# Optimization experiments

Hardware: AMD Instinct MI355X
Metric: run time of the kernel (lower is better)

The kernel has to match this reference:

```python
import jax, jax.numpy as jnp
import numpy as np

BLOCK_SIZE = 4096
EMBED_SIZE = 1024
HEAD_SIZE = 128


def setup_inputs() -> dict:
    key = jax.random.key(0)
    kx, kq, kk, kv = jax.random.split(key, 4)
    B, T = 8, BLOCK_SIZE
    x = jax.random.normal(kx, (B, T, EMBED_SIZE), dtype=jnp.float32)
    # nn.Linear(embed, head, bias=False): weight (head, embed); y = x @ W.T
    scale = 1.0 / np.sqrt(EMBED_SIZE)
    Wq = jax.random.uniform(kq, (HEAD_SIZE, EMBED_SIZE), dtype=jnp.float32, minval=-scale, maxval=scale)
    Wk = jax.random.uniform(kk, (HEAD_SIZE, EMBED_SIZE), dtype=jnp.float32, minval=-scale, maxval=scale)
    Wv = jax.random.uniform(kv, (HEAD_SIZE, EMBED_SIZE), dtype=jnp.float32, minval=-scale, maxval=scale)
    return {"x": x, "Wq": Wq, "Wk": Wk, "Wv": Wv}


def reference(x, Wq, Wk, Wv):
    B, T, C = x.shape
    q = jnp.einsum('btc,hc->bth', x, Wq)  # (B,T,H)
    k = jnp.einsum('btc,hc->bth', x, Wk)
    v = jnp.einsum('btc,hc->bth', x, Wv)
    scale = jnp.asarray(Wq.shape[0], x.dtype) ** -0.5
    wei = jnp.einsum('bth,bsh->bts', q, k) * scale  # (B,T,T)
    causal = jnp.tril(jnp.ones((T, T), dtype=bool))
    wei = jnp.where(causal, wei, -jnp.inf)
    wei = jax.nn.softmax(wei, axis=-1)
    out = jnp.einsum('bts,bsh->bth', wei, v)  # (B,T,H)
    return out
```

## Files before the change

### kernel.cpp

```cpp
#include <hip/hip_runtime.h>
#include <stdint.h>

typedef unsigned short u16;
typedef __attribute__((ext_vector_type(8))) short short8;
typedef __attribute__((ext_vector_type(4))) float f32x4;

#define B_ 8
#define T_ 4096
#define C_ 1024
#define H_ 128

#if __has_builtin(__builtin_amdgcn_exp2f)
#define EXP2(x) __builtin_amdgcn_exp2f(x)
#else
#define EXP2(x) exp2f(x)
#endif

__device__ __forceinline__ u16 f2bf(float f) {
  union { float f; uint32_t u; } v; v.f = f;
  uint32_t r = v.u + 0x7fffu + ((v.u >> 16) & 1u);
  return (u16)(r >> 16);
}

__device__ __forceinline__ void gl_lds16(const u16* g, u16* l) {
  __builtin_amdgcn_global_load_lds(
      (const __attribute__((address_space(1))) void*)g,
      (__attribute__((address_space(3))) void*)l, 16, 0, 0);
}

__global__ __launch_bounds__(256) void wconv_kernel(
    const float* __restrict__ Wq, const float* __restrict__ Wk,
    const float* __restrict__ Wv, u16* __restrict__ Wb) {
  int g = (blockIdx.x * 256 + threadIdx.x) * 8;
  int head = g >> 17;
  int off  = g & 131071;
  const float* W = (head == 0) ? Wq : (head == 1) ? Wk : Wv;
  float s = (head == 0) ? 0.08838834764831845f : 1.0f;
  float4 a = *(const float4*)(W + off);
  float4 b = *(const float4*)(W + off + 4);
  u16 o[8] = {f2bf(a.x * s), f2bf(a.y * s), f2bf(a.z * s), f2bf(a.w * s),
              f2bf(b.x * s), f2bf(b.y * s), f2bf(b.z * s), f2bf(b.w * s)};
  *(uint4*)(Wb + g) = *(const uint4*)o;
}

__global__ __launch_bounds__(512) void proj_kernel(
    const float* __restrict__ x, const u16* __restrict__ Wb,
    u16* __restrict__ qo, u16* __restrict__ ko, u16* __restrict__ vto) {
  __shared__ u16 Xl[64 * 72];
  __shared__ u16 Wl[384 * 72];

  const int bm   = blockIdx.x;
  const int tid  = threadIdx.x;
  const int wave = tid >> 6;
  const int lane = tid & 63;
  const int m    = lane & 15;
  const int q4   = lane >> 4;
  const int rowg = wave & 1;
  const int colg = wave >> 1;

  f32x4 acc[12] = {};

  const int xrow = tid >> 3, xc8 = (tid & 7) * 8;

  for (int kc = 0; kc < C_; kc += 64) {
    __syncthreads();
    {
      const float* xp = x + (size_t)(bm * 64 + xrow) * C_ + kc + xc8;
      float4 a = *(const float4*)xp;
      float4 b = *(const float4*)(xp + 4);
      u16 o[8] = {f2bf(a.x), f2bf(a.y), f2bf(a.z), f2bf(a.w),
                  f2bf(b.x), f2bf(b.y), f2bf(b.z), f2bf(b.w)};
      *(uint4*)&Xl[xrow * 72 + xc8] = *(const uint4*)o;
    }
    #pragma unroll
    for (int i = 0; i < 6; ++i) {
      int g = i * 512 + tid;
      int row = g >> 3, c8 = (g & 7) * 8;
      *(uint4*)&Wl[row * 72 + c8] =
          *(const uint4*)(Wb + (size_t)row * C_ + kc + c8);
    }
    __syncthreads();

    #pragma unroll
    for (int kb = 0; kb < 2; ++kb) {
      short8 af0 = *(const short8*)&Xl[(rowg * 32 + m) * 72 + kb * 32 + q4 * 8];
      short8 af1 = *(const short8*)&Xl[(rowg * 32 + 16 + m) * 72 + kb * 32 + q4 * 8];
      #pragma unroll
      for (int nb = 0; nb < 6; ++nb) {
        short8 bf = *(const short8*)&Wl[(colg * 96 + nb * 16 + m) * 72 + kb * 32 + q4 * 8];
        acc[nb]     = __builtin_amdgcn_mfma_f32_16x16x32_bf16(af0, bf, acc[nb], 0, 0, 0);
        acc[6 + nb] = __builtin_amdgcn_mfma_f32_16x16x32_bf16(af1, bf, acc[6 + nb], 0, 0, 0);
      }
    }
  }

  #pragma unroll
  for (int half = 0; half < 2; ++half) {
    const int rowoff = rowg * 32 + half * 16 + q4 * 4;
    #pragma unroll
    for (int nb = 0; nb < 6; ++nb) {
      int col = colg * 96 + nb * 16 + m;
      f32x4 a = acc[half * 6 + nb];
      if (col < 128) {
        #pragma unroll
        for (int r = 0; r < 4; ++r)
          qo[(size_t)(bm * 64 + rowoff + r) * H_ + col] = f2bf(a[r]);
      } else if (col < 256) {
        #pragma unroll
        for (int r = 0; r < 4; ++r)
          ko[(size_t)(bm * 64 + rowoff + r) * H_ + (col - 128)] = f2bf(a[r]);
      } else {
        int b = bm >> 6;
        int t = (bm & 63) * 64 + rowoff;
        u16* vp = vto + (size_t)b * H_ * T_ + (size_t)(col - 256) * T_ + t;
        #pragma unroll
        for (int r = 0; r < 4; ++r) vp[r] = f2bf(a[r]);
      }
    }
  }
}

__global__ __launch_bounds__(256, 2) void attn_kernel(
    const u16* __restrict__ q, const u16* __restrict__ k,
    const u16* __restrict__ vt, float* __restrict__ out,
    float* __restrict__ po, float* __restrict__ pl) {
  __shared__ u16 Kl[2][64 * 128];
  __shared__ u16 Vl[2][128 * 64];
  __shared__ u16 Pl[4][16 * 72];

  const int bid   = blockIdx.x;
  const int batch = bid & 7;
  const int c     = bid >> 3;
  int qt, ck;
  if (c < 64)       { qt = 63 - (c >> 2);         ck = c & 3; }
  else if (c < 112) { qt = 47 - (c - 64) / 3;     ck = (c - 64) % 3; }
  else if (c < 144) { qt = 31 - ((c - 112) >> 1); ck = (c - 112) & 1; }
  else              { qt = 15 - (c - 144);        ck = 0; }
  const int k0   = ck * 16;
  const int kend = min(k0 + 16, qt + 1);
  const bool single = (qt < 16);

  const int tid  = threadIdx.x;
  const int wave = tid >> 6;
  const int lane = tid & 63;
  const int m    = lane & 15;
  const int q4   = lane >> 4;

  const size_t bbase = (size_t)batch * T_ * H_;
  const u16* vbase   = vt + (size_t)batch * H_ * T_;

  short8 qf[4];
  {
    const u16* qp = q + bbase + (size_t)(qt * 64 + wave * 16 + m) * H_;
    #pragma unroll
    for (int kb = 0; kb < 4; ++kb)
      qf[kb] = *(const short8*)(qp + kb * 32 + q4 * 8);
  }

  const u16* gK[4];
  const u16* gV[4];
  #pragma unroll
  for (int j = 0; j < 4; ++j) {
    int r = wave * 16 + j * 4 + (lane >> 4);
    gK[j] = k + bbase + (size_t)r * H_ + (((lane & 15) ^ (r & 7)) << 3);
    int h = wave * 32 + j * 8 + (lane >> 3);
    gV[j] = vbase + (size_t)h * T_ + (((lane & 7) ^ (h & 7)) << 3);
  }

#define STAGE(bi, KT)                                                         \
  {                                                                           \
    u16* kd = &Kl[bi][wave * 16 * 128];                                       \
    const size_t ko_ = (size_t)(KT) * (64 * H_);                              \
    _Pragma("unroll") for (int j = 0; j < 4; ++j)                             \
        gl_lds16(gK[j] + ko_, kd + j * 4 * 128);                              \
    u16* vd = &Vl[bi][wave * 32 * 64];                                        \
    const size_t vo_ = (size_t)(KT) * 64;                                     \
    _Pragma("unroll") for (int j = 0; j < 4; ++j)                             \
        gl_lds16(gV[j] + vo_, vd + j * 8 * 64);                               \
  }

  float li[4] = {0.f, 0.f, 0.f, 0.f};
  f32x4 o[8] = {};
  const float L2E = 1.4426950408889634f;
  const float NEGINF = -__builtin_inff();

  STAGE(0, k0);
  __syncthreads();
  int cur = 0;

  for (int kt = k0; kt < kend; ++kt) {
    if (kt + 1 < kend) STAGE(cur ^ 1, kt + 1);

    f32x4 s[4];
    __builtin_amdgcn_s_setprio(1);
    #pragma unroll
    for (int nb = 0; nb < 4; ++nb) {
      f32x4 a = {};
      #pragma unroll
      for (int kb = 0; kb < 4; ++kb) {
        short8 kf = *(const short8*)&Kl[cur][(nb * 16 + m) * 128 +
                                             (((kb * 4 + q4) ^ (m & 7)) << 3)];
        a = __builtin_amdgcn_mfma_f32_16x16x32_bf16(qf[kb], kf, a, 0, 0, 0);
      }
      s[nb] = a;
    }
    __builtin_amdgcn_s_setprio(0);

    if (kt == qt) {
      #pragma unroll
      for (int nb = 0; nb < 4; ++nb)
        #pragma unroll
        for (int r = 0; r < 4; ++r) {
          int col = nb * 16 + m;
          int row = wave * 16 + q4 * 4 + r;
          if (col > row) s[nb][r] = NEGINF;
        }
    }

    #pragma unroll
    for (int nb = 0; nb < 4; ++nb)
      #pragma unroll
      for (int r = 0; r < 4; ++r) {
        float p = EXP2(s[nb][r] * L2E);
        li[r] += p;
        Pl[wave][(q4 * 4 + r) * 72 + nb * 16 + m] = f2bf(p);
      }

    __asm__ __volatile__("s_waitcnt lgkmcnt(0)" ::: "memory");

    __builtin_amdgcn_s_setprio(1);
    #pragma unroll
    for (int kb2 = 0; kb2 < 2; ++kb2) {
      short8 pf = *(const short8*)&Pl[wave][m * 72 + kb2 * 32 + q4 * 8];
      #pragma unroll
      for (int nb = 0; nb < 8; ++nb) {
        short8 vf = *(const short8*)&Vl[cur][(nb * 16 + m) * 64 +
                                             (((kb2 * 4 + q4) ^ (m & 7)) << 3)];
        o[nb] = __builtin_amdgcn_mfma_f32_16x16x32_bf16(pf, vf, o[nb], 0, 0, 0);
      }
    }
    __builtin_amdgcn_s_setprio(0);

    if (kt + 1 < kend) {
      __syncthreads();
      cur ^= 1;
    }
  }

  #pragma unroll
  for (int r = 0; r < 4; ++r) {
    float t0 = li[r];
    t0 += __shfl_xor(t0, 1, 64);
    t0 += __shfl_xor(t0, 2, 64);
    t0 += __shfl_xor(t0, 4, 64);
    t0 += __shfl_xor(t0, 8, 64);
    li[r] = t0;
  }

  if (single) {
    float* op = out + bbase + (size_t)(qt * 64 + wave * 16) * H_;
    #pragma unroll
    for (int nb = 0; nb < 8; ++nb)
      #pragma unroll
      for (int r = 0; r < 4; ++r)
        op[(q4 * 4 + r) * H_ + nb * 16 + m] = o[nb][r] / li[r];
  } else {
    const size_t slot = (size_t)(batch * 64 + qt) * 4 + ck;
    float* pp = po + (slot * 64 + wave * 16) * 128;
    #pragma unroll
    for (int nb = 0; nb < 8; ++nb)
      #pragma unroll
      for (int r = 0; r < 4; ++r)
        pp[(q4 * 4 + r) * 128 + nb * 16 + m] = o[nb][r];
    if (m == 0) {
      #pragma unroll
      for (int r = 0; r < 4; ++r)
        pl[slot * 64 + wave * 16 + q4 * 4 + r] = li[r];
    }
  }
}

__global__ __launch_bounds__(256) void combine_kernel(
    const float* __restrict__ po, const float* __restrict__ pl,
    float* __restrict__ out) {
  int gid = blockIdx.x * 256 + threadIdx.x;
  int h4  = (gid & 31) * 4;
  int tt  = (gid >> 5) & 4095;
  int b   = gid >> 17;
  int qt  = tt >> 6, row = tt & 63;
  if (qt < 16) return;
  int nc = (qt >> 4) + 1;
  float4 s = {0.f, 0.f, 0.f, 0.f};
  float l = 0.f;
  for (int ck = 0; ck < nc; ++ck) {
    size_t slot = (size_t)(b * 64 + qt) * 4 + ck;
    float4 p = *(const float4*)(po + (slot * 64 + row) * 128 + h4);
    s.x += p.x; s.y += p.y; s.z += p.z; s.w += p.w;
    l += pl[slot * 64 + row];
  }
  float inv = 1.0f / l;
  float4 r; r.x = s.x * inv; r.y = s.y * inv; r.z = s.z * inv; r.w = s.w * inv;
  *(float4*)(out + ((size_t)b * T_ + tt) * H_ + h4) = r;
}

extern "C" void kernel_launch(void* const* d_in, const int* in_sizes, int n_in,
                              void* d_out, int out_size, void* d_ws,
                              size_t ws_size, hipStream_t stream) {
  const float* x  = (const float*)d_in[0];
  const float* Wq = (const float*)d_in[1];
  const float* Wk = (const float*)d_in[2];
  const float* Wv = (const float*)d_in[3];

  const size_t n = (size_t)B_ * T_ * H_;
  u16* qb  = (u16*)d_ws;
  u16* kb  = qb + n;
  u16* vtb = kb + n;
  u16* Wbb = vtb + n;
  float* po = (float*)(Wbb + 393216);
  float* pl = po + (size_t)512 * 4 * 64 * 128;

  wconv_kernel<<<dim3(192), dim3(256), 0, stream>>>(Wq, Wk, Wv, Wbb);
  proj_kernel<<<dim3(512), dim3(512), 0, stream>>>(x, Wbb, qb, kb, vtb);
  attn_kernel<<<dim3(1280), dim3(256), 0, stream>>>(qb, kb, vtb, (float*)d_out, po, pl);
  combine_kernel<<<dim3(4096), dim3(256), 0, stream>>>(po, pl, (float*)d_out);
}
```

Baseline: 308.4 us.

## Double query tile to 128 rows per block, folding log2e into Wq scale

```diff
diff --git a/kernel.cpp b/kernel.cpp
--- a/kernel.cpp
+++ b/kernel.cpp
@@ -20,6 +20,11 @@
   union { float f; uint32_t u; } v; v.f = f;
   uint32_t r = v.u + 0x7fffu + ((v.u >> 16) & 1u);
   return (u16)(r >> 16);
+}
+
+__device__ __forceinline__ u16 f2bf_rn(float f) {
+  union { float f; uint32_t u; } v; v.f = f;
+  return (u16)((v.u + 0x8000u) >> 16);
 }
 
 __device__ __forceinline__ void gl_lds16(const u16* g, u16* l) {
@@ -35,7 +40,7 @@
   int head = g >> 17;
   int off  = g & 131071;
   const float* W = (head == 0) ? Wq : (head == 1) ? Wk : Wv;
-  float s = (head == 0) ? 0.08838834764831845f : 1.0f;
+  float s = (head == 0) ? 0.12751743342f : 1.0f;
   float4 a = *(const float4*)(W + off);
   float4 b = *(const float4*)(W + off + 4);
   u16 o[8] = {f2bf(a.x * s), f2bf(a.y * s), f2bf(a.z * s), f2bf(a.w * s),
@@ -126,19 +131,20 @@
     float* __restrict__ po, float* __restrict__ pl) {
   __shared__ u16 Kl[2][64 * 128];
   __shared__ u16 Vl[2][128 * 64];
-  __shared__ u16 Pl[4][16 * 72];
+  __shared__ u16 Pl[4][2][16 * 64];
 
   const int bid   = blockIdx.x;
   const int batch = bid & 7;
   const int c     = bid >> 3;
-  int qt, ck;
-  if (c < 64)       { qt = 63 - (c >> 2);         ck = c & 3; }
-  else if (c < 112) { qt = 47 - (c - 64) / 3;     ck = (c - 64) % 3; }
-  else if (c < 144) { qt = 31 - ((c - 112) >> 1); ck = (c - 112) & 1; }
-  else              { qt = 15 - (c - 144);        ck = 0; }
+  int Q, ck;
+  if (c < 24)      { Q = 31 - c / 3;        ck = c % 3; }
+  else if (c < 40) { Q = 23 - (c - 24) / 2; ck = (c - 24) & 1; }
+  else if (c < 48) { Q = 15 - (c - 40);     ck = 0; }
+  else { int t = c - 48; int qm = 7 - (t >> 2);
+         Q = qm + (t & 3) * 8; ck = Q >> 3; }
   const int k0   = ck * 16;
-  const int kend = min(k0 + 16, qt + 1);
-  const bool single = (qt < 16);
+  const int kend = min(k0 + 16, 2 * Q + 2);
+  const bool single = (Q < 8);
 
   const int tid  = threadIdx.x;
   const int wave = tid >> 6;
@@ -149,12 +155,13 @@
   const size_t bbase = (size_t)batch * T_ * H_;
   const u16* vbase   = vt + (size_t)batch * H_ * T_;
 
-  short8 qf[4];
-  {
-    const u16* qp = q + bbase + (size_t)(qt * 64 + wave * 16 + m) * H_;
+  short8 qf[2][4];
+  #pragma unroll
+  for (int si = 0; si < 2; ++si) {
+    const u16* qp = q + bbase + (size_t)(Q * 128 + wave * 32 + si * 16 + m) * H_;
     #pragma unroll
     for (int kb = 0; kb < 4; ++kb)
-      qf[kb] = *(const short8*)(qp + kb * 32 + q4 * 8);
+      qf[si][kb] = *(const short8*)(qp + kb * 32 + q4 * 8);
   }
 
   const u16* gK[4];
@@ -179,9 +186,8 @@
         gl_lds16(gV[j] + vo_, vd + j * 8 * 64);                               \
   }
 
-  float li[4] = {0.f, 0.f, 0.f, 0.f};
-  f32x4 o[8] = {};
-  const float L2E = 1.4426950408889634f;
+  float li[2][4] = {};
+  f32x4 o[2][8] = {};
   const float NEGINF = -__builtin_inff();
 
   STAGE(0, k0);
@@ -191,52 +197,64 @@
   for (int kt = k0; kt < kend; ++kt) {
     if (kt + 1 < kend) STAGE(cur ^ 1, kt + 1);
 
-    f32x4 s[4];
+    f32x4 sv[2][4];
     __builtin_amdgcn_s_setprio(1);
     #pragma unroll
     for (int nb = 0; nb < 4; ++nb) {
-      f32x4 a = {};
+      f32x4 a0 = {}, a1 = {};
       #pragma unroll
       for (int kb = 0; kb < 4; ++kb) {
         short8 kf = *(const short8*)&Kl[cur][(nb * 16 + m) * 128 +
                                              (((kb * 4 + q4) ^ (m & 7)) << 3)];
-        a = __builtin_amdgcn_mfma_f32_16x16x32_bf16(qf[kb], kf, a, 0, 0, 0);
-      }
-      s[nb] = a;
+        a0 = __builtin_amdgcn_mfma_f32_16x16x32_bf16(qf[0][kb], kf, a0, 0, 0, 0);
+        a1 = __builtin_amdgcn_mfma_f32_16x16x32_bf16(qf[1][kb], kf, a1, 0, 0, 0);
+      }
+      sv[0][nb] = a0; sv[1][nb] = a1;
     }
     __builtin_amdgcn_s_setprio(0);
 
-    if (kt == qt) {
+    if ((kt >> 1) == Q) {
+      #pragma unroll
+      for (int si = 0; si < 2; ++si)
+        #pragma unroll
+        for (int nb = 0; nb < 4; ++nb)
+          #pragma unroll
+          for (int r = 0; r < 4; ++r) {
+            int key = ((kt & 1) << 6) + nb * 16 + m;
+            int row = wave * 32 + si * 16 + q4 * 4 + r;
+            if (key > row) sv[si][nb][r] = NEGINF;
+          }
+    }
+
+    #pragma unroll
+    for (int si = 0; si < 2; ++si)
       #pragma unroll
       for (int nb = 0; nb < 4; ++nb)
         #pragma unroll
         for (int r = 0; r < 4; ++r) {
-          int col = nb * 16 + m;
-          int row = wave * 16 + q4 * 4 + r;
-          if (col > row) s[nb][r] = NEGINF;
+          float p = EXP2(sv[si][nb][r]);
+          li[si][r] += p;
+          int rr = q4 * 4 + r;
+          Pl[wave][si][rr * 64 + (((nb * 2 + (m >> 3)) ^ (rr & 7)) << 3) +
+                       (m & 7)] = f2bf_rn(p);
         }
-    }
-
-    #pragma unroll
-    for (int nb = 0; nb < 4; ++nb)
-      #pragma unroll
-      for (int r = 0; r < 4; ++r) {
-        float p = EXP2(s[nb][r] * L2E);
-        li[r] += p;
-        Pl[wave][(q4 * 4 + r) * 72 + nb * 16 + m] = f2bf(p);
-      }
 
     __asm__ __volatile__("s_waitcnt lgkmcnt(0)" ::: "memory");
+    __builtin_amdgcn_sched_barrier(0);
 
     __builtin_amdgcn_s_setprio(1);
     #pragma unroll
     for (int kb2 = 0; kb2 < 2; ++kb2) {
-      short8 pf = *(const short8*)&Pl[wave][m * 72 + kb2 * 32 + q4 * 8];
+      short8 pf0 = *(const short8*)&Pl[wave][0][m * 64 +
+                                   (((kb2 * 4 + q4) ^ (m & 7)) << 3)];
+      short8 pf1 = *(const short8*)&Pl[wave][1][m * 64 +
+                                   (((kb2 * 4 + q4) ^ (m & 7)) << 3)];
       #pragma unroll
       for (int nb = 0; nb < 8; ++nb) {
         short8 vf = *(const short8*)&Vl[cur][(nb * 16 + m) * 64 +
                                              (((kb2 * 4 + q4) ^ (m & 7)) << 3)];
-        o[nb] = __builtin_amdgcn_mfma_f32_16x16x32_bf16(pf, vf, o[nb], 0, 0, 0);
+        o[0][nb] = __builtin_amdgcn_mfma_f32_16x16x32_bf16(pf0, vf, o[0][nb], 0, 0, 0);
+        o[1][nb] = __builtin_amdgcn_mfma_f32_16x16x32_bf16(pf1, vf, o[1][nb], 0, 0, 0);
       }
     }
     __builtin_amdgcn_s_setprio(0);
@@ -248,34 +266,42 @@
   }
 
   #pragma unroll
-  for (int r = 0; r < 4; ++r) {
-    float t0 = li[r];
-    t0 += __shfl_xor(t0, 1, 64);
-    t0 += __shfl_xor(t0, 2, 64);
-    t0 += __shfl_xor(t0, 4, 64);
-    t0 += __shfl_xor(t0, 8, 64);
-    li[r] = t0;
-  }
+  for (int si = 0; si < 2; ++si)
+    #pragma unroll
+    for (int r = 0; r < 4; ++r) {
+      float t0 = li[si][r];
+      t0 += __shfl_xor(t0, 1, 64);
+      t0 += __shfl_xor(t0, 2, 64);
+      t0 += __shfl_xor(t0, 4, 64);
+      t0 += __shfl_xor(t0, 8, 64);
+      li[si][r] = t0;
+    }
 
   if (single) {
-    float* op = out + bbase + (size_t)(qt * 64 + wave * 16) * H_;
-    #pragma unroll
-    for (int nb = 0; nb < 8; ++nb)
-      #pragma unroll
-      for (int r = 0; r < 4; ++r)
-        op[(q4 * 4 + r) * H_ + nb * 16 + m] = o[nb][r] / li[r];
+    #pragma unroll
+    for (int si = 0; si < 2; ++si) {
+      float* op = out + bbase + (size_t)(Q * 128 + wave * 32 + si * 16) * H_;
+      #pragma unroll
+      for (int nb = 0; nb < 8; ++nb)
+        #pragma unroll
+        for (int r = 0; r < 4; ++r)
+          op[(q4 * 4 + r) * H_ + nb * 16 + m] = o[si][nb][r] / li[si][r];
+    }
   } else {
-    const size_t slot = (size_t)(batch * 64 + qt) * 4 + ck;
-    float* pp = po + (slot * 64 + wave * 16) * 128;
-    #pragma unroll
-    for (int nb = 0; nb < 8; ++nb)
-      #pragma unroll
-      for (int r = 0; r < 4; ++r)
-        pp[(q4 * 4 + r) * 128 + nb * 16 + m] = o[nb][r];
-    if (m == 0) {
-      #pragma unroll
-      for (int r = 0; r < 4; ++r)
-        pl[slot * 64 + wave * 16 + q4 * 4 + r] = li[r];
+    const size_t slot = (size_t)(batch * 32 + Q) * 4 + ck;
+    #pragma unroll
+    for (int si = 0; si < 2; ++si) {
+      float* pp = po + slot * 16384 + (size_t)(wave * 32 + si * 16) * 128;
+      #pragma unroll
+      for (int nb = 0; nb < 8; ++nb)
+        #pragma unroll
+        for (int r = 0; r < 4; ++r)
+          pp[(q4 * 4 + r) * 128 + nb * 16 + m] = o[si][nb][r];
+      if (m == 0) {
+        #pragma unroll
+        for (int r = 0; r < 4; ++r)
+          pl[slot * 128 + wave * 32 + si * 16 + q4 * 4 + r] = li[si][r];
+      }
     }
   }
 }
@@ -287,16 +313,16 @@
   int h4  = (gid & 31) * 4;
   int tt  = (gid >> 5) & 4095;
   int b   = gid >> 17;
-  int qt  = tt >> 6, row = tt & 63;
-  if (qt < 16) return;
-  int nc = (qt >> 4) + 1;
+  int Q   = tt >> 7, row = tt & 127;
+  if (Q < 8) return;
+  int nc = (Q >> 3) + 1;
   float4 s = {0.f, 0.f, 0.f, 0.f};
   float l = 0.f;
   for (int ck = 0; ck < nc; ++ck) {
-    size_t slot = (size_t)(b * 64 + qt) * 4 + ck;
-    float4 p = *(const float4*)(po + (slot * 64 + row) * 128 + h4);
+    size_t slot = (size_t)(b * 32 + Q) * 4 + ck;
+    float4 p = *(const float4*)(po + slot * 16384 + row * 128 + h4);
     s.x += p.x; s.y += p.y; s.z += p.z; s.w += p.w;
-    l += pl[slot * 64 + row];
+    l += pl[slot * 128 + row];
   }
   float inv = 1.0f / l;
   float4 r; r.x = s.x * inv; r.y = s.y * inv; r.z = s.z * inv; r.w = s.w * inv;
@@ -317,10 +343,10 @@
   u16* vtb = kb + n;
   u16* Wbb = vtb + n;
   float* po = (float*)(Wbb + 393216);
-  float* pl = po + (size_t)512 * 4 * 64 * 128;
+  float* pl = po + (size_t)1024 * 16384;
 
   wconv_kernel<<<dim3(192), dim3(256), 0, stream>>>(Wq, Wk, Wv, Wbb);
   proj_kernel<<<dim3(512), dim3(512), 0, stream>>>(x, Wbb, qb, kb, vtb);
-  attn_kernel<<<dim3(1280), dim3(256), 0, stream>>>(qb, kb, vtb, (float*)d_out, po, pl);
+  attn_kernel<<<dim3(640), dim3(256), 0, stream>>>(qb, kb, vtb, (float*)d_out, po, pl);
   combine_kernel<<<dim3(4096), dim3(256), 0, stream>>>(po, pl, (float*)d_out);
 }
```

Result: faster. 279.2 us (-9.5%).
